# Kernel optimization log

Measured on AMD Instinct MI355X. Metric: run time of the kernel, lower is better.

## Reference

```python
import jax, jax.numpy as jnp
import numpy as np


def setup_inputs() -> dict:
    key = jax.random.key(0)
    ks = jax.random.split(key, 6)
    B, S, H, O, E = 4, 2048, 4096, 4096, 4
    x = jax.random.normal(ks[0], (B, S, H), dtype=jnp.float32)
    weight = jax.random.normal(ks[1], (O, H), dtype=jnp.float32)
    bias = jax.random.normal(ks[2], (O,), dtype=jnp.float32)
    gate_w = jax.random.normal(ks[3], (E, H), dtype=jnp.float32) * 0.02
    in_channel_scale = jax.random.normal(ks[4], (E, H), dtype=jnp.float32)
    out_channel_scale = jax.random.normal(ks[5], (E, O), dtype=jnp.float32)
    return {"x": x, "weight": weight, "bias": bias, "gate_w": gate_w,
            "in_channel_scale": in_channel_scale, "out_channel_scale": out_channel_scale}


def reference(x, weight, bias, gate_w, in_channel_scale, out_channel_scale):
    *lead, H = x.shape
    O = weight.shape[0]
    xf = x.reshape(-1, H)                                   # [N, H]
    # gating: Linear(H, E, bias=False) -> softmax in fp32, cast back
    router_logits = xf @ gate_w.T                           # [N, E]
    routing_weights = jax.nn.softmax(router_logits.astype(jnp.float32), axis=1).astype(x.dtype)
    in_scale = routing_weights @ in_channel_scale           # [N, H]
    out_scale = routing_weights @ out_channel_scale         # [N, O]
    bin_w = jnp.sign(weight)                                # STE sign forward
    y = ((xf * in_scale) @ bin_w.T) * out_scale + bias      # [N, O]
    return y.reshape(*lead, O)
```

## Files before the change

kernel.cpp:

```cpp
#include <hip/hip_runtime.h>
#include <hip/hip_bf16.h>

#define H_DIM 4096
#define O_DIM 4096
#define N_ROWS 8192

typedef __bf16 bf16x8 __attribute__((ext_vector_type(8)));
typedef float  f32x4  __attribute__((ext_vector_type(4)));

__device__ __forceinline__ unsigned short f32_bf16_rne(float f) {
    unsigned int u = __builtin_bit_cast(unsigned int, f);
    u += 0x7FFFu + ((u >> 16) & 1u);
    return (unsigned short)(u >> 16);
}

__device__ __forceinline__ void gload_lds16(const unsigned short* g, unsigned short* l) {
    __builtin_amdgcn_global_load_lds((const __attribute__((address_space(1))) void*)g,
                                     (__attribute__((address_space(3))) void*)l,
                                     16, 0, 0);
}

__global__ void __launch_bounds__(256) sign_kernel(const float* __restrict__ w,
                                                   unsigned short* __restrict__ bw) {
    size_t i = ((size_t)blockIdx.x * 256 + threadIdx.x) * 4;
    float4 v = *reinterpret_cast<const float4*>(w + i);
    ushort4 o;
    o.x = v.x > 0.f ? 0x3F80 : (v.x < 0.f ? 0xBF80 : 0);
    o.y = v.y > 0.f ? 0x3F80 : (v.y < 0.f ? 0xBF80 : 0);
    o.z = v.z > 0.f ? 0x3F80 : (v.z < 0.f ? 0xBF80 : 0);
    o.w = v.w > 0.f ? 0x3F80 : (v.w < 0.f ? 0xBF80 : 0);
    *reinterpret_cast<ushort4*>(bw + i) = o;
}

__global__ void __launch_bounds__(256) route_scale_kernel(
    const float* __restrict__ x, const float* __restrict__ gate_w,
    const float* __restrict__ ics, float* __restrict__ rw_out,
    unsigned short* __restrict__ xs_out)
{
    __shared__ float red[4][4];
    const int n = blockIdx.x;
    const int t = threadIdx.x;
    const float* xr = x + (size_t)n * H_DIM;

    float4 xv[4];
    float lg[4] = {0.f, 0.f, 0.f, 0.f};
#pragma unroll
    for (int c = 0; c < 4; ++c) {
        const int idx = c * 1024 + t * 4;
        xv[c] = *reinterpret_cast<const float4*>(xr + idx);
#pragma unroll
        for (int e = 0; e < 4; ++e) {
            float4 g = *reinterpret_cast<const float4*>(gate_w + e * H_DIM + idx);
            lg[e] += xv[c].x * g.x + xv[c].y * g.y + xv[c].z * g.z + xv[c].w * g.w;
        }
    }
#pragma unroll
    for (int e = 0; e < 4; ++e) {
#pragma unroll
        for (int off = 1; off < 64; off <<= 1)
            lg[e] += __shfl_xor(lg[e], off, 64);
    }
    if ((t & 63) == 0) {
        const int w = t >> 6;
        red[w][0] = lg[0]; red[w][1] = lg[1]; red[w][2] = lg[2]; red[w][3] = lg[3];
    }
    __syncthreads();
    const float l0 = red[0][0] + red[1][0] + red[2][0] + red[3][0];
    const float l1 = red[0][1] + red[1][1] + red[2][1] + red[3][1];
    const float l2 = red[0][2] + red[1][2] + red[2][2] + red[3][2];
    const float l3 = red[0][3] + red[1][3] + red[2][3] + red[3][3];
    const float m  = fmaxf(fmaxf(l0, l1), fmaxf(l2, l3));
    const float p0 = expf(l0 - m), p1 = expf(l1 - m), p2 = expf(l2 - m), p3 = expf(l3 - m);
    const float inv = 1.f / (p0 + p1 + p2 + p3);
    const float w0 = p0 * inv, w1 = p1 * inv, w2 = p2 * inv, w3 = p3 * inv;
    if (t == 0) {
        float4 wv = make_float4(w0, w1, w2, w3);
        *reinterpret_cast<float4*>(rw_out + (size_t)n * 4) = wv;
    }
#pragma unroll
    for (int c = 0; c < 4; ++c) {
        const int idx = c * 1024 + t * 4;
        float4 i0 = *reinterpret_cast<const float4*>(ics + 0 * H_DIM + idx);
        float4 i1 = *reinterpret_cast<const float4*>(ics + 1 * H_DIM + idx);
        float4 i2 = *reinterpret_cast<const float4*>(ics + 2 * H_DIM + idx);
        float4 i3 = *reinterpret_cast<const float4*>(ics + 3 * H_DIM + idx);
        const float sx = w0 * i0.x + w1 * i1.x + w2 * i2.x + w3 * i3.x;
        const float sy = w0 * i0.y + w1 * i1.y + w2 * i2.y + w3 * i3.y;
        const float sz = w0 * i0.z + w1 * i1.z + w2 * i2.z + w3 * i3.z;
        const float sw = w0 * i0.w + w1 * i1.w + w2 * i2.w + w3 * i3.w;
        ushort4 o;
        o.x = f32_bf16_rne(xv[c].x * sx);
        o.y = f32_bf16_rne(xv[c].y * sy);
        o.z = f32_bf16_rne(xv[c].z * sz);
        o.w = f32_bf16_rne(xv[c].w * sw);
        *reinterpret_cast<ushort4*>(xs_out + (size_t)n * H_DIM + idx) = o;
    }
}

__global__ void __launch_bounds__(512, 2) gemm_bin_kernel(
    const unsigned short* __restrict__ xs,
    const unsigned short* __restrict__ bw,
    const float* __restrict__ rw,
    const float* __restrict__ ocs,
    const float* __restrict__ bias,
    float* __restrict__ out)
{
    __shared__ __align__(16) char lds[131072];

    const int t  = threadIdx.x;
    const int wv = t >> 6;
    const int ln = t & 63;
    const int wr = wv >> 2;
    const int wc = wv & 3;

    const int bid = blockIdx.x;
    const int swz = (bid & 7) * 64 + (bid >> 3);
    const int rowBase = (swz >> 4) * 256;
    const int colBase = (swz & 15) * 256;

    const int s_r  = t >> 2;
    const int s_cl = (t & 3) ^ ((t >> 3) & 3);
    const unsigned short* gA = xs + (size_t)(rowBase + s_r) * H_DIM + s_cl * 8;
    const unsigned short* gB = bw + (size_t)(colBase + s_r) * H_DIM + s_cl * 8;
    char* ldsW = lds + wv * 1024;

    int aOff[8], bOff[4];
#pragma unroll
    for (int fr = 0; fr < 8; ++fr) {
        const int row = wr * 128 + fr * 16 + (ln & 15);
        aOff[fr] = row * 64 + (((ln >> 4) ^ ((row >> 1) & 3)) << 4);
    }
#pragma unroll
    for (int ni = 0; ni < 4; ++ni) {
        const int row = wc * 64 + ni * 16 + (ln & 15);
        bOff[ni] = row * 64 + (((ln >> 4) ^ ((row >> 1) & 3)) << 4);
    }

    f32x4 acc[8][4];
#pragma unroll
    for (int i = 0; i < 8; ++i)
#pragma unroll
        for (int j = 0; j < 4; ++j) acc[i][j] = (f32x4){0.f, 0.f, 0.f, 0.f};

#pragma unroll
    for (int kt = 0; kt < 3; ++kt) {
        char* sA = lds + kt * 16384;
        char* sB = lds + 65536 + kt * 16384;
#pragma unroll
        for (int j = 0; j < 2; ++j) {
            gload_lds16(gA + ((size_t)j * 128) * H_DIM + kt * 32,
                        (unsigned short*)(sA + j * 8192 + wv * 1024));
            gload_lds16(gB + ((size_t)j * 128) * H_DIM + kt * 32,
                        (unsigned short*)(sB + j * 8192 + wv * 1024));
        }
    }
    asm volatile("s_waitcnt vmcnt(8)" ::: "memory");
    __builtin_amdgcn_s_barrier();

    for (int kt = 0; kt < 128; ++kt) {
        const int sb = (kt & 3) * 16384;
        bf16x8 av[8], bv[4];
#pragma unroll
        for (int fr = 0; fr < 8; ++fr)
            av[fr] = *reinterpret_cast<const bf16x8*>(lds + sb + aOff[fr]);
#pragma unroll
        for (int ni = 0; ni < 4; ++ni)
            bv[ni] = *reinterpret_cast<const bf16x8*>(lds + 65536 + sb + bOff[ni]);

        if (kt + 3 < 128) {
            const int ks = kt + 3;
            char* sA = lds + (ks & 3) * 16384;
            char* sB = lds + 65536 + (ks & 3) * 16384;
#pragma unroll
            for (int j = 0; j < 2; ++j) {
                gload_lds16(gA + ((size_t)j * 128) * H_DIM + ks * 32,
                            (unsigned short*)(sA + j * 8192 + wv * 1024));
                gload_lds16(gB + ((size_t)j * 128) * H_DIM + ks * 32,
                            (unsigned short*)(sB + j * 8192 + wv * 1024));
            }
        }

        __builtin_amdgcn_s_setprio(1);
#pragma unroll
        for (int fr = 0; fr < 8; ++fr)
#pragma unroll
            for (int ni = 0; ni < 4; ++ni)
                acc[fr][ni] = __builtin_amdgcn_mfma_f32_16x16x32_bf16(av[fr], bv[ni], acc[fr][ni], 0, 0, 0);
        __builtin_amdgcn_s_setprio(0);

        if (kt < 125)       asm volatile("s_waitcnt vmcnt(8)" ::: "memory");
        else if (kt == 125) asm volatile("s_waitcnt vmcnt(4)" ::: "memory");
        else if (kt == 126) asm volatile("s_waitcnt vmcnt(0)" ::: "memory");
        if (kt < 127) __builtin_amdgcn_s_barrier();
    }

    float oce[4][4], bve[4];
    int cole[4];
#pragma unroll
    for (int ni = 0; ni < 4; ++ni) {
        const int col = colBase + wc * 64 + ni * 16 + (ln & 15);
        cole[ni] = col;
        oce[ni][0] = ocs[0 * O_DIM + col];
        oce[ni][1] = ocs[1 * O_DIM + col];
        oce[ni][2] = ocs[2 * O_DIM + col];
        oce[ni][3] = ocs[3 * O_DIM + col];
        bve[ni] = bias[col];
    }
#pragma unroll
    for (int fr = 0; fr < 8; ++fr) {
        float4 rwv[4];
        int rowe[4];
#pragma unroll
        for (int j = 0; j < 4; ++j) {
            const int row = rowBase + wr * 128 + fr * 16 + (ln >> 4) * 4 + j;
            rowe[j] = row;
            rwv[j] = *reinterpret_cast<const float4*>(rw + (size_t)row * 4);
        }
#pragma unroll
        for (int ni = 0; ni < 4; ++ni) {
#pragma unroll
            for (int j = 0; j < 4; ++j) {
                const float os = rwv[j].x * oce[ni][0] + rwv[j].y * oce[ni][1] +
                                 rwv[j].z * oce[ni][2] + rwv[j].w * oce[ni][3];
                out[(size_t)rowe[j] * O_DIM + cole[ni]] = acc[fr][ni][j] * os + bve[ni];
            }
        }
    }
}

extern "C" void kernel_launch(void* const* d_in, const int* in_sizes, int n_in,
                              void* d_out, int out_size, void* d_ws, size_t ws_size,
                              hipStream_t stream) {
    const float* x      = (const float*)d_in[0];
    const float* weight = (const float*)d_in[1];
    const float* bias   = (const float*)d_in[2];
    const float* gate_w = (const float*)d_in[3];
    const float* ics    = (const float*)d_in[4];
    const float* ocs    = (const float*)d_in[5];
    float* out = (float*)d_out;

    unsigned short* xs = (unsigned short*)d_ws;
    unsigned short* bw = xs + (size_t)N_ROWS * H_DIM;
    float* rw = (float*)(bw + (size_t)O_DIM * H_DIM);

    sign_kernel<<<(O_DIM * H_DIM) / (256 * 4), 256, 0, stream>>>(weight, bw);
    route_scale_kernel<<<N_ROWS, 256, 0, stream>>>(x, gate_w, ics, rw, xs);
    gemm_bin_kernel<<<(N_ROWS / 256) * (O_DIM / 256), 512, 0, stream>>>(xs, bw, rw, ocs, bias, out);
}
```

Baseline: 319.9 us.

## Double-buffer LDS fragment reads in registers across GEMM k-steps

The main k-loop is unrolled by two and uses two register sets for the A and B fragments. Each step now loads the next tile's fragments from LDS into one set while the MFMAs run on the other, so LDS read latency can overlap with matrix math. The vmcnt waits are tightened so the next LDS tile is resident one step earlier, which leaves fewer global-to-LDS loads in flight. The second fragment set adds about 48 VGPRs per thread, which could force spills or lower occupancy under the 512-thread, 2-block launch bounds.

```diff
diff --git a/kernel.cpp b/kernel.cpp
--- a/kernel.cpp
+++ b/kernel.cpp
@@ -97,6 +97,44 @@
     }
 }
 
+
+#define GEMM_STEP(KT, AVC, BVC, AVN, BVN)                                         \
+  {                                                                               \
+    const int kt_ = (KT);                                                         \
+    if (kt_ < 127) {                                                              \
+      const int sb_ = ((kt_ + 1) & 3) * 16384;                                    \
+      _Pragma("unroll")                                                           \
+      for (int fr = 0; fr < 8; ++fr)                                              \
+        AVN[fr] = *reinterpret_cast<const bf16x8*>(lds + sb_ + aOff[fr]);         \
+      _Pragma("unroll")                                                           \
+      for (int ni = 0; ni < 4; ++ni)                                              \
+        BVN[ni] = *reinterpret_cast<const bf16x8*>(lds + 65536 + sb_ + bOff[ni]); \
+    }                                                                             \
+    if (kt_ + 3 < 128) {                                                          \
+      const int ks_ = kt_ + 3;                                                    \
+      char* sA_ = lds + (ks_ & 3) * 16384;                                        \
+      char* sB_ = lds + 65536 + (ks_ & 3) * 16384;                                \
+      _Pragma("unroll")                                                           \
+      for (int j = 0; j < 2; ++j) {                                               \
+        gload_lds16(gA + ((size_t)j * 128) * H_DIM + ks_ * 32,                    \
+                    (unsigned short*)(sA_ + j * 8192 + wv * 1024));               \
+        gload_lds16(gB + ((size_t)j * 128) * H_DIM + ks_ * 32,                    \
+                    (unsigned short*)(sB_ + j * 8192 + wv * 1024));               \
+      }                                                                           \
+    }                                                                             \
+    __builtin_amdgcn_s_setprio(1);                                                \
+    _Pragma("unroll")                                                             \
+    for (int fr = 0; fr < 8; ++fr)                                                \
+      _Pragma("unroll")                                                           \
+      for (int ni = 0; ni < 4; ++ni)                                              \
+        acc[fr][ni] = __builtin_amdgcn_mfma_f32_16x16x32_bf16(AVC[fr], BVC[ni],   \
+                                                              acc[fr][ni], 0, 0, 0); \
+    __builtin_amdgcn_s_setprio(0);                                                \
+    if (kt_ <= 124)      asm volatile("s_waitcnt vmcnt(4)" ::: "memory");         \
+    else if (kt_ == 125) asm volatile("s_waitcnt vmcnt(0)" ::: "memory");         \
+    if (kt_ < 127) __builtin_amdgcn_s_barrier();                                  \
+  }
+
 __global__ void __launch_bounds__(512, 2) gemm_bin_kernel(
     const unsigned short* __restrict__ xs,
     const unsigned short* __restrict__ bw,
@@ -122,7 +160,6 @@
     const int s_cl = (t & 3) ^ ((t >> 3) & 3);
     const unsigned short* gA = xs + (size_t)(rowBase + s_r) * H_DIM + s_cl * 8;
     const unsigned short* gB = bw + (size_t)(colBase + s_r) * H_DIM + s_cl * 8;
-    char* ldsW = lds + wv * 1024;
 
     int aOff[8], bOff[4];
 #pragma unroll
@@ -154,44 +191,20 @@
                         (unsigned short*)(sB + j * 8192 + wv * 1024));
         }
     }
-    asm volatile("s_waitcnt vmcnt(8)" ::: "memory");
+    asm volatile("s_waitcnt vmcnt(4)" ::: "memory");
     __builtin_amdgcn_s_barrier();
 
-    for (int kt = 0; kt < 128; ++kt) {
-        const int sb = (kt & 3) * 16384;
-        bf16x8 av[8], bv[4];
-#pragma unroll
-        for (int fr = 0; fr < 8; ++fr)
-            av[fr] = *reinterpret_cast<const bf16x8*>(lds + sb + aOff[fr]);
-#pragma unroll
-        for (int ni = 0; ni < 4; ++ni)
-            bv[ni] = *reinterpret_cast<const bf16x8*>(lds + 65536 + sb + bOff[ni]);
-
-        if (kt + 3 < 128) {
-            const int ks = kt + 3;
-            char* sA = lds + (ks & 3) * 16384;
-            char* sB = lds + 65536 + (ks & 3) * 16384;
-#pragma unroll
-            for (int j = 0; j < 2; ++j) {
-                gload_lds16(gA + ((size_t)j * 128) * H_DIM + ks * 32,
-                            (unsigned short*)(sA + j * 8192 + wv * 1024));
-                gload_lds16(gB + ((size_t)j * 128) * H_DIM + ks * 32,
-                            (unsigned short*)(sB + j * 8192 + wv * 1024));
-            }
-        }
-
-        __builtin_amdgcn_s_setprio(1);
-#pragma unroll
-        for (int fr = 0; fr < 8; ++fr)
-#pragma unroll
-            for (int ni = 0; ni < 4; ++ni)
-                acc[fr][ni] = __builtin_amdgcn_mfma_f32_16x16x32_bf16(av[fr], bv[ni], acc[fr][ni], 0, 0, 0);
-        __builtin_amdgcn_s_setprio(0);
-
-        if (kt < 125)       asm volatile("s_waitcnt vmcnt(8)" ::: "memory");
-        else if (kt == 125) asm volatile("s_waitcnt vmcnt(4)" ::: "memory");
-        else if (kt == 126) asm volatile("s_waitcnt vmcnt(0)" ::: "memory");
-        if (kt < 127) __builtin_amdgcn_s_barrier();
+    bf16x8 avA[8], bvA[4], avB[8], bvB[4];
+#pragma unroll
+    for (int fr = 0; fr < 8; ++fr)
+        avA[fr] = *reinterpret_cast<const bf16x8*>(lds + aOff[fr]);
+#pragma unroll
+    for (int ni = 0; ni < 4; ++ni)
+        bvA[ni] = *reinterpret_cast<const bf16x8*>(lds + 65536 + bOff[ni]);
+
+    for (int kt = 0; kt < 128; kt += 2) {
+        GEMM_STEP(kt,     avA, bvA, avB, bvB);
+        GEMM_STEP(kt + 1, avB, bvB, avA, bvA);
     }
 
     float oce[4][4], bve[4];
```

Result: no change. 316.0 us (-1.2%).

## Restructure binary GEMM main loop into 8-phase ping-pong pipeline with K=64 tiles

Applied to the files above, without the earlier changes.

Replaces the 4-stage K=32 LDS ring with a double-buffered K=64 layout, using a new 128-byte-row XOR swizzle. Each iteration is split into eight MFMA phases, each covering a quarter of the output tile, with half-tile global-to-LDS stages interleaved between them. Barriers, lgkmcnt waits and sched_barriers bracket each MFMA cluster. The aim is finer-grained overlap of LDS reads, global loads and MFMA work, and fewer loop iterations. In exchange it adds many more barriers per tile, and the hand-tuned vmcnt accounting is fragile.

```diff
diff --git a/kernel.cpp b/kernel.cpp
--- a/kernel.cpp
+++ b/kernel.cpp
@@ -97,6 +97,44 @@
     }
 }
 
+
+#define LD8(OFF) (*reinterpret_cast<const bf16x8*>(lds + (OFF)))
+
+#define READ_A(FH, SB)                                                          \
+  _Pragma("unroll") for (int f_ = 0; f_ < 4; ++f_) {                            \
+    Av[f_*2+0] = LD8((SB) + aB0 + ((FH)*4 + f_) * 2048);                        \
+    Av[f_*2+1] = LD8((SB) + aB1 + ((FH)*4 + f_) * 2048);                        \
+  }
+
+#define READ_B(SET, NH, SB)                                                     \
+  _Pragma("unroll") for (int n_ = 0; n_ < 2; ++n_) {                            \
+    SET[n_*2+0] = LD8((SB) + bB0 + ((NH)*2 + n_) * 2048);                       \
+    SET[n_*2+1] = LD8((SB) + bB1 + ((NH)*2 + n_) * 2048);                       \
+  }
+
+#define MFMA16(FH, NH, BS)                                                      \
+  _Pragma("unroll") for (int f_ = 0; f_ < 4; ++f_)                              \
+  _Pragma("unroll") for (int n_ = 0; n_ < 2; ++n_)                              \
+  _Pragma("unroll") for (int k_ = 0; k_ < 2; ++k_)                              \
+    acc[(FH)*4+f_][(NH)*2+n_] = __builtin_amdgcn_mfma_f32_16x16x32_bf16(        \
+        Av[f_*2+k_], BS[n_*2+k_], acc[(FH)*4+f_][(NH)*2+n_], 0, 0, 0);
+
+#define STAGE_HALF(GPTR, ISB, H_, KT)                                           \
+  { char* d_ = lds + ((KT)&1)*65536 + (ISB)*32768 + (H_)*16384 + wv*1024;       \
+    const unsigned short* s_ = (GPTR) + (size_t)((H_)*128) * H_DIM + (KT)*64;   \
+    gload_lds16(s_, (unsigned short*)d_);                                       \
+    gload_lds16(s_ + (size_t)64 * H_DIM, (unsigned short*)(d_ + 8192)); }
+
+#define PRE_MFMA                                                                \
+  __builtin_amdgcn_s_barrier();                                                 \
+  asm volatile("s_waitcnt lgkmcnt(0)" ::: "memory");                            \
+  __builtin_amdgcn_sched_barrier(0);                                            \
+  __builtin_amdgcn_s_setprio(1);
+
+#define POST_MFMA                                                               \
+  __builtin_amdgcn_s_setprio(0);                                                \
+  __builtin_amdgcn_s_barrier();
+
 __global__ void __launch_bounds__(512, 2) gemm_bin_kernel(
     const unsigned short* __restrict__ xs,
     const unsigned short* __restrict__ bw,
@@ -118,23 +156,17 @@
     const int rowBase = (swz >> 4) * 256;
     const int colBase = (swz & 15) * 256;
 
-    const int s_r  = t >> 2;
-    const int s_cl = (t & 3) ^ ((t >> 3) & 3);
+    const int s_r  = t >> 3;
+    const int s_cl = (t & 7) ^ ((t >> 3) & 7);
     const unsigned short* gA = xs + (size_t)(rowBase + s_r) * H_DIM + s_cl * 8;
     const unsigned short* gB = bw + (size_t)(colBase + s_r) * H_DIM + s_cl * 8;
-    char* ldsW = lds + wv * 1024;
-
-    int aOff[8], bOff[4];
-#pragma unroll
-    for (int fr = 0; fr < 8; ++fr) {
-        const int row = wr * 128 + fr * 16 + (ln & 15);
-        aOff[fr] = row * 64 + (((ln >> 4) ^ ((row >> 1) & 3)) << 4);
-    }
-#pragma unroll
-    for (int ni = 0; ni < 4; ++ni) {
-        const int row = wc * 64 + ni * 16 + (ln & 15);
-        bOff[ni] = row * 64 + (((ln >> 4) ^ ((row >> 1) & 3)) << 4);
-    }
+
+    const int sw0 = (((ln >> 4) ^ (ln & 7)) << 4);
+    const int sw1 = (((4 | (ln >> 4)) ^ (ln & 7)) << 4);
+    const int aB0 = wr * 16384 + (ln & 15) * 128 + sw0;
+    const int aB1 = wr * 16384 + (ln & 15) * 128 + sw1;
+    const int bB0 = 32768 + (wc >> 1) * 16384 + (wc & 1) * 8192 + (ln & 15) * 128 + sw0;
+    const int bB1 = 32768 + (wc >> 1) * 16384 + (wc & 1) * 8192 + (ln & 15) * 128 + sw1;
 
     f32x4 acc[8][4];
 #pragma unroll
@@ -142,56 +174,50 @@
 #pragma unroll
         for (int j = 0; j < 4; ++j) acc[i][j] = (f32x4){0.f, 0.f, 0.f, 0.f};
 
-#pragma unroll
-    for (int kt = 0; kt < 3; ++kt) {
-        char* sA = lds + kt * 16384;
-        char* sB = lds + 65536 + kt * 16384;
-#pragma unroll
-        for (int j = 0; j < 2; ++j) {
-            gload_lds16(gA + ((size_t)j * 128) * H_DIM + kt * 32,
-                        (unsigned short*)(sA + j * 8192 + wv * 1024));
-            gload_lds16(gB + ((size_t)j * 128) * H_DIM + kt * 32,
-                        (unsigned short*)(sB + j * 8192 + wv * 1024));
-        }
-    }
+    bf16x8 Av[8], Ba[4], Bb[4];
+
+    STAGE_HALF(gA, 0, 0, 0); STAGE_HALF(gA, 0, 1, 0);
+    STAGE_HALF(gB, 1, 0, 0); STAGE_HALF(gB, 1, 1, 0);
+    STAGE_HALF(gA, 0, 0, 1); STAGE_HALF(gA, 0, 1, 1);
+    STAGE_HALF(gB, 1, 0, 1); STAGE_HALF(gB, 1, 1, 1);
     asm volatile("s_waitcnt vmcnt(8)" ::: "memory");
     __builtin_amdgcn_s_barrier();
 
-    for (int kt = 0; kt < 128; ++kt) {
-        const int sb = (kt & 3) * 16384;
-        bf16x8 av[8], bv[4];
-#pragma unroll
-        for (int fr = 0; fr < 8; ++fr)
-            av[fr] = *reinterpret_cast<const bf16x8*>(lds + sb + aOff[fr]);
-#pragma unroll
-        for (int ni = 0; ni < 4; ++ni)
-            bv[ni] = *reinterpret_cast<const bf16x8*>(lds + 65536 + sb + bOff[ni]);
-
-        if (kt + 3 < 128) {
-            const int ks = kt + 3;
-            char* sA = lds + (ks & 3) * 16384;
-            char* sB = lds + 65536 + (ks & 3) * 16384;
-#pragma unroll
-            for (int j = 0; j < 2; ++j) {
-                gload_lds16(gA + ((size_t)j * 128) * H_DIM + ks * 32,
-                            (unsigned short*)(sA + j * 8192 + wv * 1024));
-                gload_lds16(gB + ((size_t)j * 128) * H_DIM + ks * 32,
-                            (unsigned short*)(sB + j * 8192 + wv * 1024));
-            }
-        }
-
-        __builtin_amdgcn_s_setprio(1);
-#pragma unroll
-        for (int fr = 0; fr < 8; ++fr)
-#pragma unroll
-            for (int ni = 0; ni < 4; ++ni)
-                acc[fr][ni] = __builtin_amdgcn_mfma_f32_16x16x32_bf16(av[fr], bv[ni], acc[fr][ni], 0, 0, 0);
-        __builtin_amdgcn_s_setprio(0);
-
-        if (kt < 125)       asm volatile("s_waitcnt vmcnt(8)" ::: "memory");
-        else if (kt == 125) asm volatile("s_waitcnt vmcnt(4)" ::: "memory");
-        else if (kt == 126) asm volatile("s_waitcnt vmcnt(0)" ::: "memory");
-        if (kt < 127) __builtin_amdgcn_s_barrier();
+    for (int it = 0; it < 32; ++it) {
+        const int T1 = 2 * it + 1, T2 = 2 * it + 2, T3 = 2 * it + 3;
+
+        READ_A(0, 0); READ_B(Ba, 0, 0);
+        if (it >= 1) STAGE_HALF(gA, 0, 0, T1);
+        PRE_MFMA; MFMA16(0, 0, Ba); POST_MFMA;
+
+        READ_B(Bb, 1, 0);
+        if (it >= 1) STAGE_HALF(gA, 0, 1, T1);
+        PRE_MFMA; MFMA16(0, 1, Bb); POST_MFMA;
+
+        READ_A(1, 0);
+        if (it < 31) STAGE_HALF(gB, 1, 0, T2);
+        PRE_MFMA; MFMA16(1, 1, Bb); POST_MFMA;
+
+        if (it < 31) STAGE_HALF(gB, 1, 1, T2);
+        if (it < 31) asm volatile("s_waitcnt vmcnt(4)" ::: "memory");
+        else         asm volatile("s_waitcnt vmcnt(0)" ::: "memory");
+        PRE_MFMA; MFMA16(1, 0, Ba); POST_MFMA;
+
+        READ_A(0, 65536); READ_B(Ba, 0, 65536);
+        if (it < 31) STAGE_HALF(gA, 0, 0, T2);
+        PRE_MFMA; MFMA16(0, 0, Ba); POST_MFMA;
+
+        READ_B(Bb, 1, 65536);
+        if (it < 31) STAGE_HALF(gA, 0, 1, T2);
+        PRE_MFMA; MFMA16(0, 1, Bb); POST_MFMA;
+
+        READ_A(1, 65536);
+        if (it < 31) STAGE_HALF(gB, 1, 0, T3);
+        PRE_MFMA; MFMA16(1, 1, Bb); POST_MFMA;
+
+        if (it < 31) STAGE_HALF(gB, 1, 1, T3);
+        if (it < 31) asm volatile("s_waitcnt vmcnt(4)" ::: "memory");
+        PRE_MFMA; MFMA16(1, 0, Ba); POST_MFMA;
     }
 
     float oce[4][4], bve[4];
```

Measured after the change: 314.9 us. About the same (-1.5%).
